# Optimization experiments

Measured on AMD Instinct MI355X. Metric: run time of the kernel, lower is better.

## Reference

```python
import jax, jax.numpy as jnp
import numpy as np

B, MPG, TPG = 64, 32, 8192          # graphs, machines/graph, tasks/graph
NM, NT = B * MPG, B * TPG           # total machines, total tasks
NL, H, DT, DM = 65536, 64, 18, 8    # labels, hidden, task feat dim, machine feat dim
TASK_FEAT_IDX = 0

PNAMES = ["t_ln_g", "t_ln_b", "t_w1", "t_b1", "t_w2", "t_b2",
          "m_ln_g", "m_ln_b", "m_w1", "m_b1", "m_w2", "m_b2",
          "a_w1", "a_b1", "a_w2", "a_b2",
          "lg_w1", "lg_b1", "lg_w2", "lg_b2",
          "o_w1", "o_b1", "o_w2", "o_b2"]

def _ln(x, g, b, eps=1e-5):
    mu = jnp.mean(x, -1, keepdims=True)
    var = jnp.mean((x - mu) ** 2, -1, keepdims=True)
    return (x - mu) * jax.lax.rsqrt(var + eps) * g + b

def _mlp(x, w1, b1, w2, b2):  # Linear -> ReLU -> Linear
    return jax.nn.relu(x @ w1 + b1) @ w2 + b2

def _seg_mean(x, seg, n):
    s = jax.ops.segment_sum(x, seg, num_segments=n)
    c = jax.ops.segment_sum(jnp.ones((x.shape[0],), x.dtype), seg, num_segments=n)
    return s / jnp.maximum(c, 1.0)[:, None]

def setup_inputs():
    key = jax.random.key(0)
    ks = jax.random.split(key, 16)
    x_tasks = jax.random.normal(ks[0], (NT, DT), jnp.float32)
    assign = jax.random.randint(ks[1], (NT,), -1, MPG).astype(jnp.float32)
    x_tasks = x_tasks.at[:, TASK_FEAT_IDX].set(assign)  # machine assignment feature, -1 = unassigned
    x_machines = jax.random.normal(ks[2], (NM, DM), jnp.float32)
    x_tasks_batch = (jnp.arange(NT) // TPG).astype(jnp.int32)
    x_machines_batch = (jnp.arange(NM) // MPG).astype(jnp.int32)
    task_label_idx = jax.random.randint(ks[3], (NL,), 0, NT).astype(jnp.int32)
    def lin(k, i, o):
        s = 1.0 / np.sqrt(i)
        kw, kb = jax.random.split(k)
        return (jax.random.uniform(kw, (i, o), jnp.float32, -s, s),
                jax.random.uniform(kb, (o,), jnp.float32, -s, s))
    p = {}
    p["t_ln_g"], p["t_ln_b"] = jnp.ones((DT,), jnp.float32), jnp.zeros((DT,), jnp.float32)
    p["m_ln_g"], p["m_ln_b"] = jnp.ones((DM,), jnp.float32), jnp.zeros((DM,), jnp.float32)
    p["t_w1"], p["t_b1"] = lin(ks[4], DT, H)
    p["t_w2"], p["t_b2"] = lin(ks[5], H, H)
    p["m_w1"], p["m_b1"] = lin(ks[6], DM, H)
    p["m_w2"], p["m_b2"] = lin(ks[7], H, H)
    p["a_w1"], p["a_b1"] = lin(ks[8], 2 * H, H)
    p["a_w2"], p["a_b2"] = lin(ks[9], H, H)
    p["lg_w1"], p["lg_b1"] = lin(ks[10], 3 * H, H)
    p["lg_w2"], p["lg_b2"] = lin(ks[11], H, H)
    p["o_w1"], p["o_b1"] = lin(ks[12], H, H)
    p["o_w2"], p["o_b2"] = lin(ks[13], H, 1)
    return {"x_tasks": x_tasks, "x_machines": x_machines,
            "x_tasks_batch": x_tasks_batch, "x_machines_batch": x_machines_batch,
            "task_label_idx": task_label_idx, **p}

def _forward(x_tasks, x_machines, x_tasks_batch, x_machines_batch, task_label_idx, p):
    # tasks_select_assignment: per-graph machine idx -> global machine idx; -1 -> padding row NM
    assign = x_tasks[:, TASK_FEAT_IDX].astype(jnp.int32)
    counts = jax.ops.segment_sum(jnp.ones((NM,), jnp.float32), x_machines_batch, num_segments=B)
    cum = (jnp.cumsum(counts) - counts).astype(jnp.int32)  # exclusive cumsum of machine counts
    task_m = jnp.where(assign == -1, NM, assign + cum[x_tasks_batch])
    th = _mlp(_ln(x_tasks, p["t_ln_g"], p["t_ln_b"]), p["t_w1"], p["t_b1"], p["t_w2"], p["t_b2"])
    mh = _mlp(_ln(x_machines, p["m_ln_g"], p["m_ln_b"]), p["m_w1"], p["m_b1"], p["m_w2"], p["m_b2"])
    aggr = _mlp(jnp.concatenate([_seg_mean(th, x_tasks_batch, B),
                                 _seg_mean(mh, x_machines_batch, B)], axis=1),
                p["a_w1"], p["a_b1"], p["a_w2"], p["a_b2"])
    mh_pad = jnp.concatenate([mh, jnp.zeros((1, H), mh.dtype)], axis=0)
    cat = jnp.concatenate([th, aggr[x_tasks_batch], mh_pad[task_m]], axis=1)  # [NT, 3H]
    hid = _mlp(cat, p["lg_w1"], p["lg_b1"], p["lg_w2"], p["lg_b2"])
    out = _mlp(hid, p["o_w1"], p["o_b1"], p["o_w2"], p["o_b2"])
    return out[task_label_idx]  # [NL, 1]

def reference(x_tasks, x_machines, x_tasks_batch, x_machines_batch, task_label_idx,
              t_ln_g, t_ln_b, t_w1, t_b1, t_w2, t_b2,
              m_ln_g, m_ln_b, m_w1, m_b1, m_w2, m_b2,
              a_w1, a_b1, a_w2, a_b2, lg_w1, lg_b1, lg_w2, lg_b2,
              o_w1, o_b1, o_w2, o_b2):
    p = dict(zip(PNAMES, (t_ln_g, t_ln_b, t_w1, t_b1, t_w2, t_b2,
                          m_ln_g, m_ln_b, m_w1, m_b1, m_w2, m_b2,
                          a_w1, a_b1, a_w2, a_b2, lg_w1, lg_b1, lg_w2, lg_b2,
                          o_w1, o_b1, o_w2, o_b2)))
    return _forward(x_tasks, x_machines, x_tasks_batch, x_machines_batch, task_label_idx, p)
```

## Files before the change

kernel.cpp:

```cpp
#include <hip/hip_runtime.h>

#define B_GRAPHS 64
#define MPG 32
#define TPG 8192
#define NM 2048
#define NT 524288
#define NL 65536
#define H 64
#define DT 18
#define DM 8

typedef __attribute__((ext_vector_type(8))) short bf8;
typedef __attribute__((ext_vector_type(4))) float f32x4;

__device__ __forceinline__ unsigned short f2bf(float f) {
    unsigned u = __builtin_bit_cast(unsigned, f);
    u += 0x7FFFu + ((u >> 16) & 1u);
    return (unsigned short)(u >> 16);
}
__device__ __forceinline__ float bf2f(unsigned short h) {
    return __builtin_bit_cast(float, (unsigned)h << 16);
}

__global__ __launch_bounds__(256) void k_front(
    const float* __restrict__ xt,
    const float* __restrict__ t_ln_g, const float* __restrict__ t_ln_b,
    const float* __restrict__ t_w1, const float* __restrict__ t_b1,
    const float* __restrict__ xm,
    const float* __restrict__ m_ln_g, const float* __restrict__ m_ln_b,
    const float* __restrict__ m_w1, const float* __restrict__ m_b1,
    const float* __restrict__ m_w2, const float* __restrict__ m_b2,
    const float* __restrict__ lg_w1,
    const float* __restrict__ t_w2, const float* __restrict__ lg_w2,
    const float* __restrict__ o_w1, const float* __restrict__ t_b2,
    const float* __restrict__ lg_b1, const float* __restrict__ lg_b2,
    const float* __restrict__ o_b1,
    float* __restrict__ t_sum_partial,
    float* __restrict__ t_cnt_partial,
    float* __restrict__ mh,
    float* __restrict__ mh_contrib,
    float* __restrict__ W_comb, float* __restrict__ W2comb,
    float* __restrict__ biasA, float* __restrict__ bias2)
{
    __shared__ float        s_stage[4608];
    __shared__ unsigned int s_pk[5152];
    __shared__ float s_part[4][64];
    __shared__ float s_h[4][64];
    __shared__ float s_m[4][64];

    int tid = threadIdx.x, lane = tid & 63, w = tid >> 6;
    int bid = blockIdx.x;

    if (bid < 512) {
        int col = lane & 15, grp = lane >> 4;
        long base = (long)bid * 1024;

        bf8 bfrag[4];
        float b1c[4];
#pragma unroll
        for (int t = 0; t < 4; t++) {
#pragma unroll
            for (int j = 0; j < 8; j++) {
                int k = grp * 8 + j;
                float wv = (k < DT) ? t_w1[k * H + t * 16 + col] : 0.0f;
                bfrag[t][j] = (short)f2bf(wv);
            }
            b1c[t] = t_b1[t * 16 + col];
        }
        float lg[DT], lb[DT];
#pragma unroll
        for (int i = 0; i < DT; i++) { lg[i] = t_ln_g[i]; lb[i] = t_ln_b[i]; }

        float colsum[4] = {0.0f, 0.0f, 0.0f, 0.0f};

#pragma unroll 1
        for (int tile = 0; tile < 4; tile++) {
            const float4* src4 = (const float4*)(xt + (base + tile * 256) * DT);
            float4* s4 = (float4*)s_stage;
#pragma unroll
            for (int r = 0; r < 4; r++) s4[r * 256 + tid] = src4[r * 256 + tid];
            if (tid < 128) s4[1024 + tid] = src4[1024 + tid];
            __syncthreads();

            const float* srow = s_stage + tid * DT;
            float xv[DT];
#pragma unroll
            for (int q = 0; q < 9; q++) {
                float2 v = *(const float2*)(srow + 2 * q);
                xv[2 * q] = v.x; xv[2 * q + 1] = v.y;
            }
            float mu = 0.0f;
#pragma unroll
            for (int i = 0; i < DT; i++) mu += xv[i];
            mu *= (1.0f / DT);
            float var = 0.0f;
#pragma unroll
            for (int i = 0; i < DT; i++) { float d = xv[i] - mu; var += d * d; }
            var *= (1.0f / DT);
            float rs = rsqrtf(var + 1e-5f);
            unsigned int pk[16];
#pragma unroll
            for (int q = 0; q < 9; q++) {
                float a0 = (xv[2 * q]     - mu) * rs * lg[2 * q]     + lb[2 * q];
                float a1 = (xv[2 * q + 1] - mu) * rs * lg[2 * q + 1] + lb[2 * q + 1];
                pk[q] = (unsigned int)f2bf(a0) | ((unsigned int)f2bf(a1) << 16);
            }
#pragma unroll
            for (int q = 9; q < 16; q++) pk[q] = 0u;

            {
                unsigned off = tid * 20u + ((tid >> 3) & 7) * 4u;
                uint4* dst = (uint4*)&s_pk[off];
                dst[0] = make_uint4(pk[0], pk[1], pk[2], pk[3]);
                dst[1] = make_uint4(pk[4], pk[5], pk[6], pk[7]);
                dst[2] = make_uint4(pk[8], pk[9], pk[10], pk[11]);
                dst[3] = make_uint4(pk[12], pk[13], pk[14], pk[15]);
            }
            __syncthreads();

#pragma unroll
            for (int s4i = 0; s4i < 4; s4i++) {
                int row = (s4i * 4 + w) * 16 + col;
                unsigned roff = (unsigned)row * 20u + (((unsigned)row >> 3) & 7) * 4u
                              + (unsigned)grp * 4u;
                bf8 a = *(const bf8*)&s_pk[roff];
#pragma unroll
                for (int t = 0; t < 4; t++) {
                    f32x4 cini = {b1c[t], b1c[t], b1c[t], b1c[t]};
                    f32x4 d = __builtin_amdgcn_mfma_f32_16x16x32_bf16(a, bfrag[t], cini, 0, 0, 0);
                    colsum[t] += (fmaxf(d[0], 0.0f) + fmaxf(d[1], 0.0f))
                               + (fmaxf(d[2], 0.0f) + fmaxf(d[3], 0.0f));
                }
            }
            __syncthreads();
        }

#pragma unroll
        for (int t = 0; t < 4; t++) {
            colsum[t] += __shfl_xor(colsum[t], 16);
            colsum[t] += __shfl_xor(colsum[t], 32);
        }
        if (lane < 16) {
#pragma unroll
            for (int t = 0; t < 4; t++) s_part[w][t * 16 + lane] = colsum[t];
        }
        __syncthreads();
        if (tid < 64) {
            float s = s_part[0][tid] + s_part[1][tid] + s_part[2][tid] + s_part[3][tid];
            t_sum_partial[bid * 64 + tid] = s;
        }
        if (tid == 0) t_cnt_partial[bid] = 1024.0f;

    } else if (bid < 576) {
        int mbid = bid - 512;
        if (mbid == 0 && tid < 64) mh_contrib[(long)NM * H + tid] = 0.0f;

        float w1r[DM];
#pragma unroll
        for (int i = 0; i < DM; i++) w1r[i] = m_w1[i * H + lane];
        float w2r[H];
#pragma unroll
        for (int i = 0; i < H; i++) w2r[i] = m_w2[i * H + lane];
        float Cr[H];
#pragma unroll
        for (int i = 0; i < H; i++) Cr[i] = lg_w1[(2 * H + i) * H + lane];
        float b1 = m_b1[lane], b2 = m_b2[lane];
        float g0[DM], bb[DM];
#pragma unroll
        for (int i = 0; i < DM; i++) { g0[i] = m_ln_g[i]; bb[i] = m_ln_b[i]; }

        int W = mbid * 4 + w;
        for (int k = 0; k < 8; k++) {
            int m = W * 8 + k;
            float x[DM];
#pragma unroll
            for (int i = 0; i < DM; i++) x[i] = xm[m * DM + i];
            float mu = 0.0f;
#pragma unroll
            for (int i = 0; i < DM; i++) mu += x[i];
            mu *= (1.0f / DM);
            float var = 0.0f;
#pragma unroll
            for (int i = 0; i < DM; i++) { float d = x[i] - mu; var += d * d; }
            var *= (1.0f / DM);
            float rs = rsqrtf(var + 1e-5f);
            float h = b1;
#pragma unroll
            for (int i = 0; i < DM; i++) {
                float xn = (x[i] - mu) * rs * g0[i] + bb[i];
                h = fmaf(xn, w1r[i], h);
            }
            h = fmaxf(h, 0.0f);
            __syncthreads();
            s_h[w][lane] = h;
            __syncthreads();
            float o = b2;
#pragma unroll
            for (int i = 0; i < H; i++) o = fmaf(s_h[w][i], w2r[i], o);
            __syncthreads();
            s_m[w][lane] = o;
            __syncthreads();
            float c = 0.0f;
#pragma unroll
            for (int i = 0; i < H; i++) c = fmaf(s_m[w][i], Cr[i], c);
            mh[(long)m * H + lane] = o;
            mh_contrib[(long)m * H + lane] = c;
        }
    } else {
        int i = bid - 576, j = tid;
        if (j < 64) {
            float a = 0.0f, b = 0.0f;
            for (int k = 0; k < H; k++) {
                a = fmaf(t_w2[i * H + k],  lg_w1[k * H + j], a);
                b = fmaf(lg_w2[i * H + k], o_w1[k * H + j], b);
            }
            W_comb[i * H + j] = a;
            W2comb[i * H + j] = b;
            if (i == 0) {
                float ba = lg_b1[j], b2v = o_b1[j];
                for (int k = 0; k < H; k++) {
                    ba  = fmaf(t_b2[k],  lg_w1[k * H + j], ba);
                    b2v = fmaf(lg_b2[k], o_w1[k * H + j], b2v);
                }
                biasA[j] = ba;
                bias2[j] = b2v;
            }
        }
    }
}

__global__ __launch_bounds__(64) void k_graph(
    const float* __restrict__ t_sum_partial, const float* __restrict__ t_cnt_partial,
    const float* __restrict__ mh, const int* __restrict__ mbatch,
    const float* __restrict__ t_w2, const float* __restrict__ t_b2,
    const float* __restrict__ a_w1, const float* __restrict__ a_b1,
    const float* __restrict__ a_w2, const float* __restrict__ a_b2,
    const float* __restrict__ lg_w1, const float* __restrict__ biasA,
    float* __restrict__ aggr_contrib, int* __restrict__ cum)
{
    int g = blockIdx.x, j = threadIdx.x;
    __shared__ float rs_[64], tm[64], mm[64], ah[64], ag[64];
    __shared__ float s_tcnt;
    __shared__ int s_lt[64], s_eq[64];

    float s = 0.0f;
    for (int p = 0; p < 8; p++) s += t_sum_partial[(g * 8 + p) * 64 + j];
    rs_[j] = s;
    if (j == 0) {
        float c = 0.0f;
        for (int p = 0; p < 8; p++) c += t_cnt_partial[g * 8 + p];
        s_tcnt = c;
    }
    int clt = 0, ceq = 0;
    for (int k = 0; k < 32; k++) {
        int bt = mbatch[j * 32 + k];
        clt += (bt < g) ? 1 : 0;
        ceq += (bt == g) ? 1 : 0;
    }
    s_lt[j] = clt; s_eq[j] = ceq;
    float msum = 0.0f;
    for (int k = 0; k < MPG; k++) msum += mh[(long)(g * MPG + k) * H + j];
    __syncthreads();

    int cum_g = 0, mcnt = 0;
    for (int k = 0; k < 64; k++) { cum_g += s_lt[k]; mcnt += s_eq[k]; }
    if (j == 0) cum[g] = cum_g;

    float tcnt = s_tcnt;
    float dot = 0.0f;
    for (int i = 0; i < H; i++) dot = fmaf(rs_[i], t_w2[i * H + j], dot);
    tm[j] = (dot + tcnt * t_b2[j]) / fmaxf(tcnt, 1.0f);
    mm[j] = msum / fmaxf((float)mcnt, 1.0f);
    __syncthreads();

    float h = a_b1[j];
    for (int i = 0; i < H; i++) h = fmaf(tm[i], a_w1[i * H + j], h);
    for (int i = 0; i < H; i++) h = fmaf(mm[i], a_w1[(H + i) * H + j], h);
    ah[j] = fmaxf(h, 0.0f);
    __syncthreads();

    float o = a_b2[j];
    for (int i = 0; i < H; i++) o = fmaf(ah[i], a_w2[i * H + j], o);
    ag[j] = o;
    __syncthreads();

    float c = biasA[j];
    for (int i = 0; i < H; i++) c = fmaf(ag[i], lg_w1[(H + i) * H + j], c);
    aggr_contrib[g * H + j] = c;
}

__global__ __launch_bounds__(512) void k_labels_mma(
    const float* __restrict__ xt, const int* __restrict__ tbatch,
    const int* __restrict__ lidx,
    const float* __restrict__ t_ln_g, const float* __restrict__ t_ln_b,
    const float* __restrict__ t_w1, const float* __restrict__ t_b1,
    const float* __restrict__ W_comb, const float* __restrict__ W2comb,
    const float* __restrict__ bias2,
    const float* __restrict__ o_w2, const float* __restrict__ o_b2,
    const float* __restrict__ aggr_contrib, const float* __restrict__ mh_contrib,
    const int* __restrict__ cum,
    float* __restrict__ out)
{
    __shared__ float s_xn[DT * 128];
    __shared__ float s_w1[DT * H];
    __shared__ __align__(16) unsigned short s_Bhi[64 * 72];
    __shared__ __align__(16) unsigned short s_Blo[64 * 72];
    __shared__ __align__(16) unsigned short s_Ahi[128 * 72];
    __shared__ __align__(16) unsigned short s_Alo[128 * 72];
    __shared__ float s_b1v[H];
    __shared__ float s_lng[DT], s_lnb[DT];
    __shared__ int   s_gi[128], s_mi[128], s_t[128];

    int tid = threadIdx.x, lane = tid & 63, w = tid >> 6;
    int col = lane & 15, kg = lane >> 4;

    for (int i = tid; i < DT * H; i += 512) s_w1[i] = t_w1[i];
    if (tid < H) s_b1v[tid] = t_b1[tid];
    if (tid < DT) { s_lng[tid] = t_ln_g[tid]; s_lnb[tid] = t_ln_b[tid]; }
    if (tid < 128) {
        int t = lidx[blockIdx.x * 128 + tid];
        s_t[tid] = t;
        int g = tbatch[t];
        int assign = (int)xt[(long)t * DT];
        s_gi[tid] = g;
        s_mi[tid] = (assign < 0) ? NM : (assign + cum[g]);
    }
#pragma unroll
    for (int s = 0; s < 8; s++) {
        int idx = tid + s * 512;
        int i = idx >> 6, j = idx & 63;
        float v = W_comb[idx];
        unsigned short hi = f2bf(v);
        unsigned short lo = f2bf(v - bf2f(hi));
        s_Bhi[j * 72 + i] = hi;
        s_Blo[j * 72 + i] = lo;
    }
    __syncthreads();

    if (tid < 256) {
        int r = tid >> 1, hh = tid & 1;
        const float* src = xt + (long)s_t[r] * DT + hh * 9;
#pragma unroll
        for (int j = 0; j < 9; j++) s_xn[(hh * 9 + j) * 128 + r] = src[j];
    }
    __syncthreads();

    if (tid < 128) {
        float xv[DT];
#pragma unroll
        for (int i = 0; i < DT; i++) xv[i] = s_xn[i * 128 + tid];
        float mu = 0.0f;
#pragma unroll
        for (int i = 0; i < DT; i++) mu += xv[i];
        mu *= (1.0f / DT);
        float var = 0.0f;
#pragma unroll
        for (int i = 0; i < DT; i++) { float d = xv[i] - mu; var += d * d; }
        var *= (1.0f / DT);
        float rs = rsqrtf(var + 1e-5f);
#pragma unroll
        for (int i = 0; i < DT; i++)
            s_xn[i * 128 + tid] = (xv[i] - mu) * rs * s_lng[i] + s_lnb[i];
    }
    __syncthreads();

    int wb = w * 8;
    float acc0[8], acc1[8];
#pragma unroll
    for (int k = 0; k < 8; k++) { acc0[k] = s_b1v[wb + k]; acc1[k] = acc0[k]; }
    for (int i = 0; i < DT; i++) {
        float av0 = s_xn[i * 128 + lane];
        float av1 = s_xn[i * 128 + 64 + lane];
        const float4* wp = (const float4*)(s_w1 + i * H + wb);
        float4 wA = wp[0], wB = wp[1];
        acc0[0] = fmaf(av0, wA.x, acc0[0]); acc1[0] = fmaf(av1, wA.x, acc1[0]);
        acc0[1] = fmaf(av0, wA.y, acc0[1]); acc1[1] = fmaf(av1, wA.y, acc1[1]);
        acc0[2] = fmaf(av0, wA.z, acc0[2]); acc1[2] = fmaf(av1, wA.z, acc1[2]);
        acc0[3] = fmaf(av0, wA.w, acc0[3]); acc1[3] = fmaf(av1, wA.w, acc1[3]);
        acc0[4] = fmaf(av0, wB.x, acc0[4]); acc1[4] = fmaf(av1, wB.x, acc1[4]);
        acc0[5] = fmaf(av0, wB.y, acc0[5]); acc1[5] = fmaf(av1, wB.y, acc1[5]);
        acc0[6] = fmaf(av0, wB.z, acc0[6]); acc1[6] = fmaf(av1, wB.z, acc1[6]);
        acc0[7] = fmaf(av0, wB.w, acc0[7]); acc1[7] = fmaf(av1, wB.w, acc1[7]);
    }
    {
        unsigned int h0[4], l0[4], h1[4], l1[4];
#pragma unroll
        for (int q = 0; q < 4; q++) {
            float v0 = fmaxf(acc0[2 * q], 0.0f), v1 = fmaxf(acc0[2 * q + 1], 0.0f);
            unsigned short a = f2bf(v0), b = f2bf(v1);
            h0[q] = (unsigned)a | ((unsigned)b << 16);
            l0[q] = (unsigned)f2bf(v0 - bf2f(a)) | ((unsigned)f2bf(v1 - bf2f(b)) << 16);
            float u0 = fmaxf(acc1[2 * q], 0.0f), u1 = fmaxf(acc1[2 * q + 1], 0.0f);
            unsigned short c = f2bf(u0), d = f2bf(u1);
            h1[q] = (unsigned)c | ((unsigned)d << 16);
            l1[q] = (unsigned)f2bf(u0 - bf2f(c)) | ((unsigned)f2bf(u1 - bf2f(d)) << 16);
        }
        *(uint4*)&s_Ahi[lane * 72 + wb]        = make_uint4(h0[0], h0[1], h0[2], h0[3]);
        *(uint4*)&s_Alo[lane * 72 + wb]        = make_uint4(l0[0], l0[1], l0[2], l0[3]);
        *(uint4*)&s_Ahi[(64 + lane) * 72 + wb] = make_uint4(h1[0], h1[1], h1[2], h1[3]);
        *(uint4*)&s_Alo[(64 + lane) * 72 + wb] = make_uint4(l1[0], l1[1], l1[2], l1[3]);
    }
    __syncthreads();

    int labA = w * 16 + col;
    int labC = w * 16 + kg * 4;
    bf8 Ahi0 = *(const bf8*)&s_Ahi[labA * 72 + kg * 8];
    bf8 Ahi1 = *(const bf8*)&s_Ahi[labA * 72 + 32 + kg * 8];
    bf8 Alo0 = *(const bf8*)&s_Alo[labA * 72 + kg * 8];
    bf8 Alo1 = *(const bf8*)&s_Alo[labA * 72 + 32 + kg * 8];
    int gv[4], mv[4];
#pragma unroll
    for (int r = 0; r < 4; r++) { gv[r] = s_gi[labC + r]; mv[r] = s_mi[labC + r]; }

    f32x4 p1[4];
#pragma unroll
    for (int nt = 0; nt < 4; nt++) {
        int brow = nt * 16 + col;
        bf8 Bhi0 = *(const bf8*)&s_Bhi[brow * 72 + kg * 8];
        bf8 Bhi1 = *(const bf8*)&s_Bhi[brow * 72 + 32 + kg * 8];
        bf8 Blo0 = *(const bf8*)&s_Blo[brow * 72 + kg * 8];
        bf8 Blo1 = *(const bf8*)&s_Blo[brow * 72 + 32 + kg * 8];
        int dim = nt * 16 + col;
        f32x4 c;
#pragma unroll
        for (int r = 0; r < 4; r++)
            c[r] = aggr_contrib[gv[r] * H + dim] + mh_contrib[(long)mv[r] * H + dim];
        c = __builtin_amdgcn_mfma_f32_16x16x32_bf16(Alo0, Bhi0, c, 0, 0, 0);
        c = __builtin_amdgcn_mfma_f32_16x16x32_bf16(Alo1, Bhi1, c, 0, 0, 0);
        c = __builtin_amdgcn_mfma_f32_16x16x32_bf16(Ahi0, Blo0, c, 0, 0, 0);
        c = __builtin_amdgcn_mfma_f32_16x16x32_bf16(Ahi1, Blo1, c, 0, 0, 0);
        c = __builtin_amdgcn_mfma_f32_16x16x32_bf16(Ahi0, Bhi0, c, 0, 0, 0);
        c = __builtin_amdgcn_mfma_f32_16x16x32_bf16(Ahi1, Bhi1, c, 0, 0, 0);
        p1[nt] = c;
    }
    __syncthreads();

#pragma unroll
    for (int nt = 0; nt < 4; nt++) {
#pragma unroll
        for (int r = 0; r < 4; r++) {
            float v = fmaxf(p1[nt][r], 0.0f);
            unsigned short hi = f2bf(v);
            unsigned short lo = f2bf(v - bf2f(hi));
            int lab = labC + r;
            s_Ahi[lab * 72 + nt * 16 + col] = hi;
            s_Alo[lab * 72 + nt * 16 + col] = lo;
        }
    }
#pragma unroll
    for (int s = 0; s < 8; s++) {
        int idx = tid + s * 512;
        int i = idx >> 6, j = idx & 63;
        float v = W2comb[idx];
        unsigned short hi = f2bf(v);
        unsigned short lo = f2bf(v - bf2f(hi));
        s_Bhi[j * 72 + i] = hi;
        s_Blo[j * 72 + i] = lo;
    }
    __syncthreads();

    bf8 Hhi0 = *(const bf8*)&s_Ahi[labA * 72 + kg * 8];
    bf8 Hhi1 = *(const bf8*)&s_Ahi[labA * 72 + 32 + kg * 8];
    bf8 Hlo0 = *(const bf8*)&s_Alo[labA * 72 + kg * 8];
    bf8 Hlo1 = *(const bf8*)&s_Alo[labA * 72 + 32 + kg * 8];

    float sv[4] = {0.0f, 0.0f, 0.0f, 0.0f};
#pragma unroll
    for (int nt = 0; nt < 4; nt++) {
        int brow = nt * 16 + col;
        bf8 Bhi0 = *(const bf8*)&s_Bhi[brow * 72 + kg * 8];
        bf8 Bhi1 = *(const bf8*)&s_Bhi[brow * 72 + 32 + kg * 8];
        bf8 Blo0 = *(const bf8*)&s_Blo[brow * 72 + kg * 8];
        bf8 Blo1 = *(const bf8*)&s_Blo[brow * 72 + 32 + kg * 8];
        int dim = nt * 16 + col;
        float bz = bias2[dim];
        f32x4 c = {bz, bz, bz, bz};
        c = __builtin_amdgcn_mfma_f32_16x16x32_bf16(Hlo0, Bhi0, c, 0, 0, 0);
        c = __builtin_amdgcn_mfma_f32_16x16x32_bf16(Hlo1, Bhi1, c, 0, 0, 0);
        c = __builtin_amdgcn_mfma_f32_16x16x32_bf16(Hhi0, Blo0, c, 0, 0, 0);
        c = __builtin_amdgcn_mfma_f32_16x16x32_bf16(Hhi1, Blo1, c, 0, 0, 0);
        c = __builtin_amdgcn_mfma_f32_16x16x32_bf16(Hhi0, Bhi0, c, 0, 0, 0);
        c = __builtin_amdgcn_mfma_f32_16x16x32_bf16(Hhi1, Bhi1, c, 0, 0, 0);
        float ow = o_w2[dim];
#pragma unroll
        for (int r = 0; r < 4; r++)
            sv[r] = fmaf(fmaxf(c[r], 0.0f), ow, sv[r]);
    }
#pragma unroll
    for (int r = 0; r < 4; r++) {
        sv[r] += __shfl_xor(sv[r], 1);
        sv[r] += __shfl_xor(sv[r], 2);
        sv[r] += __shfl_xor(sv[r], 4);
        sv[r] += __shfl_xor(sv[r], 8);
    }
    if (col == 0) {
        float ob = o_b2[0];
#pragma unroll
        for (int r = 0; r < 4; r++)
            out[blockIdx.x * 128 + labC + r] = ob + sv[r];
    }
}

extern "C" void kernel_launch(void* const* d_in, const int* in_sizes, int n_in,
                              void* d_out, int out_size, void* d_ws, size_t ws_size,
                              hipStream_t stream)
{
    (void)n_in; (void)out_size; (void)ws_size;
    const float* x_tasks         = (const float*)d_in[0];
    const float* x_machines      = (const float*)d_in[1];
    const int*   x_tasks_batch   = (const int*)d_in[2];
    const int*   x_machines_batch= (const int*)d_in[3];
    const int*   task_label_idx  = (const int*)d_in[4];
    const float* t_ln_g = (const float*)d_in[5];
    const float* t_ln_b = (const float*)d_in[6];
    const float *m_ln_g, *m_ln_b, *t_w1, *t_b1, *t_w2, *t_b2;
    if (in_sizes[7] == DM) {
        m_ln_g = (const float*)d_in[7];  m_ln_b = (const float*)d_in[8];
        t_w1   = (const float*)d_in[9];  t_b1   = (const float*)d_in[10];
        t_w2   = (const float*)d_in[11]; t_b2   = (const float*)d_in[12];
    } else {
        t_w1   = (const float*)d_in[7];  t_b1   = (const float*)d_in[8];
        t_w2   = (const float*)d_in[9];  t_b2   = (const float*)d_in[10];
        m_ln_g = (const float*)d_in[11]; m_ln_b = (const float*)d_in[12];
    }
    const float* m_w1 = (const float*)d_in[13]; const float* m_b1 = (const float*)d_in[14];
    const float* m_w2 = (const float*)d_in[15]; const float* m_b2 = (const float*)d_in[16];
    const float* a_w1 = (const float*)d_in[17]; const float* a_b1 = (const float*)d_in[18];
    const float* a_w2 = (const float*)d_in[19]; const float* a_b2 = (const float*)d_in[20];
    const float* lg_w1= (const float*)d_in[21]; const float* lg_b1= (const float*)d_in[22];
    const float* lg_w2= (const float*)d_in[23]; const float* lg_b2= (const float*)d_in[24];
    const float* o_w1 = (const float*)d_in[25]; const float* o_b1 = (const float*)d_in[26];
    const float* o_w2 = (const float*)d_in[27]; const float* o_b2 = (const float*)d_in[28];

    float* ws = (float*)d_ws;
    float* mh_contrib    = ws;
    float* mh_arr        = ws + 131136;
    float* t_sum_partial = ws + 262208;
    float* t_cnt_partial = ws + 294976;
    float* W_comb        = ws + 295488;
    float* W2comb        = ws + 299584;
    float* biasA         = ws + 303680;
    float* bias2         = ws + 303744;
    float* aggr_contrib  = ws + 303808;
    int*   cum           = (int*)(ws + 307904);

    k_front<<<640, 256, 0, stream>>>(x_tasks, t_ln_g, t_ln_b, t_w1, t_b1,
                                     x_machines, m_ln_g, m_ln_b, m_w1, m_b1, m_w2, m_b2,
                                     lg_w1, t_w2, lg_w2, o_w1, t_b2, lg_b1, lg_b2, o_b1,
                                     t_sum_partial, t_cnt_partial, mh_arr, mh_contrib,
                                     W_comb, W2comb, biasA, bias2);
    k_graph<<<64, 64, 0, stream>>>(t_sum_partial, t_cnt_partial, mh_arr, x_machines_batch,
                                   t_w2, t_b2, a_w1, a_b1, a_w2, a_b2, lg_w1, biasA,
                                   aggr_contrib, cum);
    k_labels_mma<<<512, 512, 0, stream>>>(x_tasks, x_tasks_batch, task_label_idx,
                                          t_ln_g, t_ln_b, t_w1, t_b1, W_comb, W2comb, bias2,
                                          o_w2, o_b2, aggr_contrib, mh_contrib, cum,
                                          (float*)d_out);
}
```

Baseline: 46.36 us.

## Give each wave a private tile with register-prefetched loads and no block barriers

New measurement: 43.35 us, median of 2. -6.5%, faster.

```diff
diff --git a/kernel.cpp b/kernel.cpp
--- a/kernel.cpp
+++ b/kernel.cpp
@@ -43,7 +43,7 @@
     float* __restrict__ biasA, float* __restrict__ bias2)
 {
     __shared__ float        s_stage[4608];
-    __shared__ unsigned int s_pk[5152];
+    __shared__ unsigned int s_pk[5248];
     __shared__ float s_part[4][64];
     __shared__ float s_h[4][64];
     __shared__ float s_m[4][64];
@@ -53,7 +53,19 @@
 
     if (bid < 512) {
         int col = lane & 15, grp = lane >> 4;
-        long base = (long)bid * 1024;
+        unsigned sbase = (unsigned)w * 1152u;
+        unsigned pbase = (unsigned)w * 1312u;
+
+        long rowbase = (long)bid * 1024 + (long)w * 256;
+        const float4* src4 = (const float4*)(xt + rowbase * DT);
+
+        float4 stg0, stg1, stg2, stg3, stg4;
+        {
+            const float4* p = src4;
+            stg0 = p[lane]; stg1 = p[64 + lane];
+            stg2 = p[128 + lane]; stg3 = p[192 + lane];
+            if (lane < 32) stg4 = p[256 + lane];
+        }
 
         bf8 bfrag[4];
         float b1c[4];
@@ -74,15 +86,22 @@
         float colsum[4] = {0.0f, 0.0f, 0.0f, 0.0f};
 
 #pragma unroll 1
-        for (int tile = 0; tile < 4; tile++) {
-            const float4* src4 = (const float4*)(xt + (base + tile * 256) * DT);
-            float4* s4 = (float4*)s_stage;
-#pragma unroll
-            for (int r = 0; r < 4; r++) s4[r * 256 + tid] = src4[r * 256 + tid];
-            if (tid < 128) s4[1024 + tid] = src4[1024 + tid];
-            __syncthreads();
-
-            const float* srow = s_stage + tid * DT;
+        for (int it = 0; it < 4; it++) {
+            float4* sd = (float4*)(s_stage + sbase);
+            sd[lane] = stg0; sd[64 + lane] = stg1;
+            sd[128 + lane] = stg2; sd[192 + lane] = stg3;
+            if (lane < 32) sd[256 + lane] = stg4;
+
+            if (it < 3) {
+                const float4* p = src4 + (it + 1) * 288;
+                stg0 = p[lane]; stg1 = p[64 + lane];
+                stg2 = p[128 + lane]; stg3 = p[192 + lane];
+                if (lane < 32) stg4 = p[256 + lane];
+            }
+
+            asm volatile("s_waitcnt lgkmcnt(0)" ::: "memory");
+
+            const float* srow = s_stage + sbase + lane * DT;
             float xv[DT];
 #pragma unroll
             for (int q = 0; q < 9; q++) {
@@ -109,19 +128,19 @@
             for (int q = 9; q < 16; q++) pk[q] = 0u;
 
             {
-                unsigned off = tid * 20u + ((tid >> 3) & 7) * 4u;
+                unsigned off = pbase + (unsigned)lane * 20u + (((unsigned)lane >> 3) & 7) * 4u;
                 uint4* dst = (uint4*)&s_pk[off];
                 dst[0] = make_uint4(pk[0], pk[1], pk[2], pk[3]);
                 dst[1] = make_uint4(pk[4], pk[5], pk[6], pk[7]);
                 dst[2] = make_uint4(pk[8], pk[9], pk[10], pk[11]);
                 dst[3] = make_uint4(pk[12], pk[13], pk[14], pk[15]);
             }
-            __syncthreads();
+            asm volatile("s_waitcnt lgkmcnt(0)" ::: "memory");
 
 #pragma unroll
             for (int s4i = 0; s4i < 4; s4i++) {
-                int row = (s4i * 4 + w) * 16 + col;
-                unsigned roff = (unsigned)row * 20u + (((unsigned)row >> 3) & 7) * 4u
+                unsigned row = (unsigned)(s4i * 16 + col);
+                unsigned roff = pbase + row * 20u + ((row >> 3) & 7) * 4u
                               + (unsigned)grp * 4u;
                 bf8 a = *(const bf8*)&s_pk[roff];
 #pragma unroll
@@ -132,7 +151,6 @@
                                + (fmaxf(d[2], 0.0f) + fmaxf(d[3], 0.0f));
                 }
             }
-            __syncthreads();
         }
 
 #pragma unroll
```
